# Kernel optimization log

Hardware: AMD Instinct MI355X
Metric: run time of the kernel (lower is better)

The kernel has to match this reference:

```python
import jax, jax.numpy as jnp
import numpy as np

SUB_NO = 128
T_HIST = 100
T_DATA = 20000
SYN_B = 3
HIST_B = 3
FIX_VAR = 1.0


def _build_kern(delta, log_tau, K):
    # delta: (S,), log_tau: (B,), K: (S,B) -> kernel (S, T_HIST)
    t = jnp.maximum(jnp.arange(T_HIST, dtype=jnp.float32)[None, :] - delta[:, None], 0.0)  # (S,T)
    tt = t[:, :, None] / jnp.exp(log_tau)[None, None, :]  # (S,T,B)
    return jnp.einsum('stb,sb->st', tt * jnp.exp(-tt), K)


def setup_inputs() -> dict:
    key = jax.random.key(0)
    ks = jax.random.split(key, 5)
    S = SUB_NO
    return {
        'S_conv': jax.random.normal(ks[0], (T_DATA, S), jnp.float32),
        'Y_ancest': jax.random.normal(ks[1], (T_DATA, S), jnp.float32),
        'Z_ancest': jax.random.uniform(ks[2], (T_DATA, S), jnp.float32),
        'noise': jax.random.normal(ks[3], (T_DATA, S), jnp.float32),
        'C_den': jax.random.uniform(ks[4], (S, S), jnp.float32),
        'W_sub': jnp.ones(S, jnp.float32) * 0.25,
        'theta_syn': jnp.zeros(S, jnp.float32),
        'K_spike': jnp.ones((S, SYN_B), jnp.float32) * 0.01,
        'tau_spike': jnp.arange(1.6, 1.6 + SYN_B, dtype=jnp.float32),
        'delta_spike': jnp.zeros(S, jnp.float32),
        'theta_spike': jnp.ones(S, jnp.float32) * (-1.0),
        'W_spike': jnp.ones(S, jnp.float32) * 0.1,
        'tau_hist': jnp.arange(0.5, 0.5 + HIST_B * 0.5, 0.5, dtype=jnp.float32),
        'K_hist': jnp.zeros((S, HIST_B), jnp.float32),
        'delta_hist': jnp.zeros(S, jnp.float32),
    }


def _forward(S_conv, Y_ancest, Z_ancest, noise, C_den, W_sub, theta_syn,
             K_spike, tau_spike, delta_spike, theta_spike, W_spike,
             tau_hist, K_hist, delta_hist):
    S = SUB_NO
    # kernels, flipped as in torch (conv1d cross-correlation with flipped kernel)
    hist_kf = _build_kern(delta_hist, tau_hist, K_hist)[:, ::-1]      # (S,T_HIST)
    anc_kf = _build_kern(delta_spike, tau_spike, K_spike)[:, ::-1]    # (S,T_HIST)

    # Ancestor path has no recurrence -> hoist out of the time loop.
    # spike_ancest filtering: C_den is linear & time-independent, so project first,
    # then depthwise-convolve along time.
    Z_pad = jnp.concatenate([jnp.zeros((T_HIST, S), S_conv.dtype), Z_ancest], axis=0)  # (T+T_HIST,S)
    A = Z_pad @ C_den.T  # (T+T_HIST, S)
    conv = jax.lax.conv_general_dilated(
        A.T[None],                 # (1, S, T+T_HIST)
        anc_kf[:, None, :],        # (S, 1, T_HIST)
        window_strides=(1,), padding='VALID',
        dimension_numbers=('NCH', 'OIH', 'NCH'),
        feature_group_count=S)     # (1, S, T_DATA+1)
    filtered_ancest = conv[0].T[:T_DATA]  # (T_DATA, S)

    raw_ancest = Y_ancest @ C_den.T  # (T_DATA, S)
    base = S_conv + theta_syn + filtered_ancest + raw_ancest  # (T_DATA,S)
    sqrt_var = FIX_VAR ** 0.5

    def step(buf, inp):
        # buf: (S, T_HIST) rolling history of Z_out (most recent at index -1)
        b, n = inp
        fh = jnp.sum(buf * hist_kf, axis=1)            # grouped conv1d == per-channel dot
        x_out = jax.nn.sigmoid(b + fh)
        down = x_out * W_spike + theta_spike           # down_mu_Z_t == mu_Z_t (up_mu_Z=None)
        z_out = jax.nn.sigmoid(down + n * sqrt_var)
        buf = jnp.concatenate([buf[:, 1:], z_out[:, None]], axis=1)
        return buf, (x_out * W_sub, z_out, down)

    buf0 = jnp.zeros((S, T_HIST), S_conv.dtype)
    _, (final_Y, final_Z, mu_Z) = jax.lax.scan(step, buf0, (base, noise))
    return final_Y, final_Z, mu_Z, mu_Z


def reference(S_conv, Y_ancest, Z_ancest, noise, C_den, W_sub, theta_syn,
              K_spike, tau_spike, delta_spike, theta_spike, W_spike,
              tau_hist, K_hist, delta_hist):
    return _forward(S_conv, Y_ancest, Z_ancest, noise, C_den, W_sub, theta_syn,
                    K_spike, tau_spike, delta_spike, theta_spike, W_spike,
                    tau_hist, K_hist, delta_hist)
```

## Files before the change

kernel.cpp:

```cpp
#include <hip/hip_runtime.h>

#define T_DATA 20000
#define S_NO   128
#define T_HIST 100
#define J_PAD  104
#define NELEM  (T_DATA * S_NO)

__device__ __forceinline__ float sigm(float v) {
    return 1.0f / (1.0f + __expf(-v));
}

__device__ __forceinline__ void fma4(float4& a, float s, const float4 c) {
    a.x = fmaf(s, c.x, a.x); a.y = fmaf(s, c.y, a.y);
    a.z = fmaf(s, c.z, a.z); a.w = fmaf(s, c.w, a.w);
}

__global__ void __launch_bounds__(256) k1_prep(const float* __restrict__ C,
                        const float* __restrict__ K_spike,
                        const float* __restrict__ tau_spike,
                        const float* __restrict__ delta_spike,
                        const float* __restrict__ tau_hist,
                        const float* __restrict__ K_hist,
                        const float* __restrict__ delta_hist,
                        float* __restrict__ Ct,
                        float* __restrict__ anc_kT,
                        float* __restrict__ hist_k,
                        int* __restrict__ flag) {
    const int tid = threadIdx.x;
    const int b   = blockIdx.x;
    if (b < 16) {
#pragma unroll
        for (int i = 0; i < 4; ++i) {
            const int q = b * 1024 + i * 256 + tid;
            Ct[(q & 127) * S_NO + (q >> 7)] = C[q];
        }
        return;
    }
    const int s    = tid & 127;
    const int half = tid >> 7;
    {
        float d  = delta_spike[s];
        float i0 = __expf(-tau_spike[0]);
        float i1 = __expf(-tau_spike[1]);
        float i2 = __expf(-tau_spike[2]);
        float k0 = K_spike[s * 3 + 0], k1 = K_spike[s * 3 + 1], k2 = K_spike[s * 3 + 2];
        for (int j = half * 52; j < half * 52 + 52; ++j) {
            float v = 0.0f;
            if (j < T_HIST) {
                float t  = fmaxf((float)j - d, 0.0f);
                float x0 = t * i0, x1 = t * i1, x2 = t * i2;
                v = k0 * x0 * __expf(-x0) + k1 * x1 * __expf(-x1) + k2 * x2 * __expf(-x2);
            }
            anc_kT[j * S_NO + s] = v;
        }
    }
    {
        float d  = delta_hist[s];
        float i0 = __expf(-tau_hist[0]);
        float i1 = __expf(-tau_hist[1]);
        float i2 = __expf(-tau_hist[2]);
        float k0 = K_hist[s * 3 + 0], k1 = K_hist[s * 3 + 1], k2 = K_hist[s * 3 + 2];
        for (int j = half * 50; j < half * 50 + 50; ++j) {
            float t  = fmaxf((float)j - d, 0.0f);
            float x0 = t * i0, x1 = t * i1, x2 = t * i2;
            hist_k[s * T_HIST + j] =
                k0 * x0 * __expf(-x0) + k1 * x1 * __expf(-x1) + k2 * x2 * __expf(-x2);
        }
    }
    if (tid == 0) *flag = 0;
    __syncthreads();
    if (tid < 128) {
        if (K_hist[s * 3] != 0.0f || K_hist[s * 3 + 1] != 0.0f || K_hist[s * 3 + 2] != 0.0f)
            atomicOr(flag, 1);
    }
}

__global__ void __launch_bounds__(256) k2_gemm(const float* __restrict__ Z,
                                               const float* __restrict__ Y,
                                               const float* __restrict__ Ct,
                                               float* __restrict__ A,
                                               float* __restrict__ R) {
    __shared__ float Zt[32 * 128];
    __shared__ float Yt[32 * 128];
    const int t0  = blockIdx.x * 32;
    const int tid = threadIdx.x;
    {
        const float4* Zg = (const float4*)(Z + t0 * S_NO);
        const float4* Yg = (const float4*)(Y + t0 * S_NO);
        float4* Zl = (float4*)Zt;
        float4* Yl = (float4*)Yt;
        for (int q = tid; q < 1024; q += 256) { Zl[q] = Zg[q]; Yl[q] = Yg[q]; }
    }
    __syncthreads();
    const int sg = tid & 31;
    const int tg = tid >> 5;
    const int s0 = sg * 4;
    float4 accA[4] = {{0,0,0,0},{0,0,0,0},{0,0,0,0},{0,0,0,0}};
    float4 accR[4] = {{0,0,0,0},{0,0,0,0},{0,0,0,0},{0,0,0,0}};
    for (int k4 = 0; k4 < 32; ++k4) {
        const float4 c0 = *(const float4*)&Ct[(k4 * 4 + 0) * S_NO + s0];
        const float4 c1 = *(const float4*)&Ct[(k4 * 4 + 1) * S_NO + s0];
        const float4 c2 = *(const float4*)&Ct[(k4 * 4 + 2) * S_NO + s0];
        const float4 c3 = *(const float4*)&Ct[(k4 * 4 + 3) * S_NO + s0];
#pragma unroll
        for (int i = 0; i < 4; ++i) {
            const float4 z = *(const float4*)&Zt[(tg * 4 + i) * S_NO + k4 * 4];
            fma4(accA[i], z.x, c0); fma4(accA[i], z.y, c1);
            fma4(accA[i], z.z, c2); fma4(accA[i], z.w, c3);
            const float4 y = *(const float4*)&Yt[(tg * 4 + i) * S_NO + k4 * 4];
            fma4(accR[i], y.x, c0); fma4(accR[i], y.y, c1);
            fma4(accR[i], y.z, c2); fma4(accR[i], y.w, c3);
        }
    }
#pragma unroll
    for (int i = 0; i < 4; ++i) {
        *(float4*)&A[(t0 + tg * 4 + i) * S_NO + s0] = accA[i];
        *(float4*)&R[(t0 + tg * 4 + i) * S_NO + s0] = accR[i];
    }
}

#define K3_LOGICAL 1250
#define K3_NPER    157
#define K3_PHYS    (8 * K3_NPER)

__device__ __forceinline__ void k3_fma_chunk(const float w[15], const float kj[8],
                                             float acc[8]) {
#pragma unroll
    for (int r = 0; r < 8; ++r)
#pragma unroll
        for (int i = 0; i < 8; ++i)
            acc[i] = fmaf(kj[r], w[i + 7 - r], acc[i]);
}

__device__ __forceinline__ void conv8_guard(const float* __restrict__ A,
                                            const float* __restrict__ kT,
                                            int t0, int s, float acc[8]) {
#pragma unroll 1
    for (int c = 0; c < 13; ++c) {
        const int B = t0 - 8 * c - 8;
        float w[15], kj[8];
#pragma unroll
        for (int q = 0; q < 15; ++q) {
            const int u = B + q;
            w[q] = (u >= 0) ? A[u * S_NO + s] : 0.0f;
        }
#pragma unroll
        for (int r = 0; r < 8; ++r) kj[r] = kT[(8 * c + r) * S_NO + s];
        k3_fma_chunk(w, kj, acc);
    }
}

__global__ void __launch_bounds__(256, 4) k3_fused(const float* __restrict__ A,
                                                const float* __restrict__ anc_kT,
                                                const float* __restrict__ S_conv,
                                                const float* __restrict__ noise,
                                                const float* __restrict__ W_sub,
                                                const float* __restrict__ theta_syn,
                                                const float* __restrict__ theta_spike,
                                                const float* __restrict__ W_spike,
                                                const int* __restrict__ flag,
                                                float* __restrict__ out0,
                                                float* __restrict__ out1,
                                                float* __restrict__ out2,
                                                float* __restrict__ out3,
                                                float* __restrict__ Fws) {
    const int blk = (blockIdx.x & 7) * K3_NPER + (blockIdx.x >> 3);
    if (blk >= K3_LOGICAL) return;
    const int tid = threadIdx.x;
    const int s   = tid & 127;
    const int tg  = tid >> 7;
    const int t0  = blk * 16 + tg * 8;
    const int fl  = *flag;

    float sc[8], nz[8], rr[8];
#pragma unroll
    for (int i = 0; i < 8; ++i) {
        const int n = (t0 + i) * S_NO + s;
        sc[i] = S_conv[n];
        nz[i] = noise[n];
        rr[i] = out1[n];
    }

    float acc[8] = {0,0,0,0,0,0,0,0};
    if (t0 >= J_PAD) {
        float w[15], kj[8];
        {
            const int B = t0 - 8;
#pragma unroll
            for (int q = 0; q < 15; ++q) w[q] = A[(B + q) * S_NO + s];
#pragma unroll
            for (int r = 0; r < 8; ++r) kj[r] = anc_kT[r * S_NO + s];
            k3_fma_chunk(w, kj, acc);
        }
#pragma unroll
        for (int c = 1; c < 13; ++c) {
            const int B = t0 - 8 * c - 8;
#pragma unroll
            for (int q = 6; q >= 0; --q) w[q + 8] = w[q];
#pragma unroll
            for (int q = 0; q < 8; ++q) w[q] = A[(B + q) * S_NO + s];
#pragma unroll
            for (int r = 0; r < 8; ++r) kj[r] = anc_kT[(8 * c + r) * S_NO + s];
            k3_fma_chunk(w, kj, acc);
        }
    } else {
        conv8_guard(A, anc_kT, t0, s, acc);
    }

    if (fl == 0) {
        const float tsy = theta_syn[s], wsub = W_sub[s];
        const float wsp = W_spike[s],  tsp  = theta_spike[s];
#pragma unroll
        for (int i = 0; i < 8; ++i) {
            const int n = (t0 + i) * S_NO + s;
            const float x  = sigm(sc[i] + tsy + rr[i] + acc[i]);
            const float dn = fmaf(x, wsp, tsp);
            const float z  = sigm(dn + nz[i]);
            out0[n] = x * wsub;
            out1[n] = z;
            out2[n] = dn;
            out3[n] = dn;
        }
    } else {
#pragma unroll
        for (int i = 0; i < 8; ++i) Fws[(t0 + i) * S_NO + s] = acc[i];
    }
}

__global__ void __launch_bounds__(64) k4_scan(const float* __restrict__ S_conv,
                                              const float* __restrict__ noise,
                                              const float* __restrict__ W_sub,
                                              const float* __restrict__ theta_syn,
                                              const float* __restrict__ theta_spike,
                                              const float* __restrict__ W_spike,
                                              const float* __restrict__ hist_k,
                                              const int* __restrict__ flag,
                                              const float* __restrict__ Fws,
                                              float* __restrict__ out0,
                                              float* __restrict__ out1,
                                              float* __restrict__ out2,
                                              float* __restrict__ out3) {
    if (*flag == 0) return;
    __shared__ float zr[128];
    const int s = blockIdx.x;
    const int l = threadIdx.x;
    zr[l] = 0.0f; zr[l + 64] = 0.0f;
    const float hk0 = (l < T_HIST) ? hist_k[s * T_HIST + l] : 0.0f;
    const float hk1 = (l + 64 < T_HIST) ? hist_k[s * T_HIST + l + 64] : 0.0f;
    const float tsy = theta_syn[s], wsub = W_sub[s];
    const float wsp = W_spike[s],  tsp  = theta_spike[s];
    for (int t = 0; t < T_DATA; ++t) {
        float fh = hk0 * zr[(t - 1 - l) & 127];
        fh = fmaf(hk1, zr[(t - 65 - l) & 127], fh);
#pragma unroll
        for (int m = 1; m < 64; m <<= 1) fh += __shfl_xor(fh, m, 64);
        const int n = t * S_NO + s;
        const float basev = S_conv[n] + tsy + out1[n] + Fws[n];
        const float x  = sigm(basev + fh);
        const float dn = fmaf(x, wsp, tsp);
        const float z  = sigm(dn + noise[n]);
        if (l == 0) {
            out0[n] = x * wsub;
            out1[n] = z;
            out2[n] = dn;
            out3[n] = dn;
            zr[t & 127] = z;
        }
    }
}

extern "C" void kernel_launch(void* const* d_in, const int* in_sizes, int n_in,
                              void* d_out, int out_size, void* d_ws, size_t ws_size,
                              hipStream_t stream) {
    const float* S_conv  = (const float*)d_in[0];
    const float* Y_anc   = (const float*)d_in[1];
    const float* Z_anc   = (const float*)d_in[2];
    const float* noise   = (const float*)d_in[3];
    const float* C_den   = (const float*)d_in[4];
    const float* W_sub   = (const float*)d_in[5];
    const float* th_syn  = (const float*)d_in[6];
    const float* K_spk   = (const float*)d_in[7];
    const float* tau_spk = (const float*)d_in[8];
    const float* dl_spk  = (const float*)d_in[9];
    const float* th_spk  = (const float*)d_in[10];
    const float* W_spk   = (const float*)d_in[11];
    const float* tau_h   = (const float*)d_in[12];
    const float* K_h     = (const float*)d_in[13];
    const float* dl_h    = (const float*)d_in[14];

    float* out  = (float*)d_out;
    float* out0 = out;
    float* out1 = out + NELEM;
    float* out2 = out + 2 * NELEM;
    float* out3 = out + 3 * NELEM;

    float* ws     = (float*)d_ws;
    float* wsA    = ws;
    float* wsF    = ws + NELEM;
    float* Ct     = ws + 2 * NELEM;
    float* anc_kT = Ct + S_NO * S_NO;
    float* hist_k = anc_kT + J_PAD * S_NO;
    int*   flag   = (int*)(hist_k + S_NO * T_HIST);

    k1_prep<<<17, 256, 0, stream>>>(C_den, K_spk, tau_spk, dl_spk, tau_h, K_h, dl_h,
                                    Ct, anc_kT, hist_k, flag);
    k2_gemm<<<T_DATA / 32, 256, 0, stream>>>(Z_anc, Y_anc, Ct, wsA, out1);
    k3_fused<<<K3_PHYS, 256, 0, stream>>>(wsA, anc_kT, S_conv, noise,
                                          W_sub, th_syn, th_spk, W_spk,
                                          flag, out0, out1, out2, out3, wsF);
    k4_scan<<<S_NO, 64, 0, stream>>>(S_conv, noise, W_sub, th_syn, th_spk, W_spk,
                                     hist_k, flag, wsF, out0, out1, out2, out3);
}
```

Baseline: 162.1 us.

## Store projected ancestor matrix time-major per channel for vectorized conv loads

The GEMM kernel now writes the projected ancestor matrix transposed (channel-major with padded row stride) through an LDS staging tile, and the ancestor kernel is stored per channel. The fused conv kernel then reads contiguous float4 windows along time for each channel and processes the 104-tap filter in 32-tap chunks. This replaces scalar strided loads with vector loads and larger register reuse, but each thread reads along its own row, so lane accesses are strided across rows. It also adds an extra LDS transpose pass, two more barriers and higher register pressure in the GEMM and conv kernels.

```diff
diff --git a/kernel.cpp b/kernel.cpp
--- a/kernel.cpp
+++ b/kernel.cpp
@@ -3,7 +3,7 @@
 #define T_DATA 20000
 #define S_NO   128
 #define T_HIST 100
-#define J_PAD  104
+#define ATPAD  20032
 #define NELEM  (T_DATA * S_NO)
 
 __device__ __forceinline__ float sigm(float v) {
@@ -23,7 +23,7 @@
                         const float* __restrict__ K_hist,
                         const float* __restrict__ delta_hist,
                         float* __restrict__ Ct,
-                        float* __restrict__ anc_kT,
+                        float* __restrict__ anc_kS,
                         float* __restrict__ hist_k,
                         int* __restrict__ flag) {
     const int tid = threadIdx.x;
@@ -51,7 +51,7 @@
                 float x0 = t * i0, x1 = t * i1, x2 = t * i2;
                 v = k0 * x0 * __expf(-x0) + k1 * x1 * __expf(-x1) + k2 * x2 * __expf(-x2);
             }
-            anc_kT[j * S_NO + s] = v;
+            anc_kS[s * 104 + j] = v;
         }
     }
     {
@@ -78,10 +78,11 @@
 __global__ void __launch_bounds__(256) k2_gemm(const float* __restrict__ Z,
                                                const float* __restrict__ Y,
                                                const float* __restrict__ Ct,
-                                               float* __restrict__ A,
+                                               float* __restrict__ At,
                                                float* __restrict__ R) {
-    __shared__ float Zt[32 * 128];
-    __shared__ float Yt[32 * 128];
+    __shared__ float lds[8320];
+    float* Zt = lds;
+    float* Yt = lds + 4096;
     const int t0  = blockIdx.x * 32;
     const int tid = threadIdx.x;
     {
@@ -113,9 +114,24 @@
         }
     }
 #pragma unroll
+    for (int i = 0; i < 4; ++i)
+        *(float4*)&R[(t0 + tg * 4 + i) * S_NO + s0] = accR[i];
+    __syncthreads();
+    float* Atile = lds;
+#pragma unroll
     for (int i = 0; i < 4; ++i) {
-        *(float4*)&A[(t0 + tg * 4 + i) * S_NO + s0] = accA[i];
-        *(float4*)&R[(t0 + tg * 4 + i) * S_NO + s0] = accR[i];
+        const int tl = tg * 4 + i;
+        Atile[(s0 + 0) * 33 + tl] = accA[i].x;
+        Atile[(s0 + 1) * 33 + tl] = accA[i].y;
+        Atile[(s0 + 2) * 33 + tl] = accA[i].z;
+        Atile[(s0 + 3) * 33 + tl] = accA[i].w;
+    }
+    __syncthreads();
+    for (int q = tid; q < 1024; q += 256) {
+        const int row = q >> 3, m = q & 7;
+        const float* a = &Atile[row * 33 + 4 * m];
+        const float4 v = make_float4(a[0], a[1], a[2], a[3]);
+        *(float4*)&At[row * ATPAD + t0 + 4 * m] = v;
     }
 }
 
@@ -123,35 +139,8 @@
 #define K3_NPER    157
 #define K3_PHYS    (8 * K3_NPER)
 
-__device__ __forceinline__ void k3_fma_chunk(const float w[15], const float kj[8],
-                                             float acc[8]) {
-#pragma unroll
-    for (int r = 0; r < 8; ++r)
-#pragma unroll
-        for (int i = 0; i < 8; ++i)
-            acc[i] = fmaf(kj[r], w[i + 7 - r], acc[i]);
-}
-
-__device__ __forceinline__ void conv8_guard(const float* __restrict__ A,
-                                            const float* __restrict__ kT,
-                                            int t0, int s, float acc[8]) {
-#pragma unroll 1
-    for (int c = 0; c < 13; ++c) {
-        const int B = t0 - 8 * c - 8;
-        float w[15], kj[8];
-#pragma unroll
-        for (int q = 0; q < 15; ++q) {
-            const int u = B + q;
-            w[q] = (u >= 0) ? A[u * S_NO + s] : 0.0f;
-        }
-#pragma unroll
-        for (int r = 0; r < 8; ++r) kj[r] = kT[(8 * c + r) * S_NO + s];
-        k3_fma_chunk(w, kj, acc);
-    }
-}
-
-__global__ void __launch_bounds__(256, 4) k3_fused(const float* __restrict__ A,
-                                                const float* __restrict__ anc_kT,
+__global__ void __launch_bounds__(256, 4) k3_fused(const float* __restrict__ At,
+                                                const float* __restrict__ anc_kS,
                                                 const float* __restrict__ S_conv,
                                                 const float* __restrict__ noise,
                                                 const float* __restrict__ W_sub,
@@ -181,30 +170,35 @@
         rr[i] = out1[n];
     }
 
+    const float* Arow = At + s * ATPAD;
+    const float* Krow = anc_kS + s * 104;
     float acc[8] = {0,0,0,0,0,0,0,0};
-    if (t0 >= J_PAD) {
-        float w[15], kj[8];
-        {
-            const int B = t0 - 8;
-#pragma unroll
-            for (int q = 0; q < 15; ++q) w[q] = A[(B + q) * S_NO + s];
-#pragma unroll
-            for (int r = 0; r < 8; ++r) kj[r] = anc_kT[r * S_NO + s];
-            k3_fma_chunk(w, kj, acc);
-        }
-#pragma unroll
-        for (int c = 1; c < 13; ++c) {
-            const int B = t0 - 8 * c - 8;
-#pragma unroll
-            for (int q = 6; q >= 0; --q) w[q + 8] = w[q];
-#pragma unroll
-            for (int q = 0; q < 8; ++q) w[q] = A[(B + q) * S_NO + s];
-#pragma unroll
-            for (int r = 0; r < 8; ++r) kj[r] = anc_kT[(8 * c + r) * S_NO + s];
-            k3_fma_chunk(w, kj, acc);
-        }
-    } else {
-        conv8_guard(A, anc_kT, t0, s, acc);
+#pragma unroll
+    for (int c = 0; c < 4; ++c) {
+        const int TC   = (c < 3) ? 32 : 8;
+        const int base = t0 - 32 * c - 32;
+        float w[40];
+#pragma unroll
+        for (int m = 0; m < 10; ++m) {
+            if (c == 3 && m < 6) continue;
+            const int off = base + 4 * m;
+            const float4 v = (off >= 0) ? *(const float4*)&Arow[off]
+                                        : make_float4(0.f, 0.f, 0.f, 0.f);
+            *(float4*)&w[4 * m] = v;
+        }
+        float kt[32];
+#pragma unroll
+        for (int m = 0; m < 8; ++m) {
+            if (4 * m >= TC) continue;
+            *(float4*)&kt[4 * m] = *(const float4*)&Krow[32 * c + 4 * m];
+        }
+#pragma unroll
+        for (int r = 0; r < 32; ++r) {
+            if (r >= TC) continue;
+#pragma unroll
+            for (int i = 0; i < 8; ++i)
+                acc[i] = fmaf(kt[r], w[i + 31 - r], acc[i]);
+        }
     }
 
     if (fl == 0) {
@@ -295,17 +289,17 @@
     float* out3 = out + 3 * NELEM;
 
     float* ws     = (float*)d_ws;
-    float* wsA    = ws;
-    float* wsF    = ws + NELEM;
-    float* Ct     = ws + 2 * NELEM;
-    float* anc_kT = Ct + S_NO * S_NO;
-    float* hist_k = anc_kT + J_PAD * S_NO;
+    float* At     = ws;
+    float* wsF    = At + S_NO * ATPAD;
+    float* Ct     = wsF + NELEM;
+    float* anc_kS = Ct + S_NO * S_NO;
+    float* hist_k = anc_kS + 104 * S_NO;
     int*   flag   = (int*)(hist_k + S_NO * T_HIST);
 
     k1_prep<<<17, 256, 0, stream>>>(C_den, K_spk, tau_spk, dl_spk, tau_h, K_h, dl_h,
-                                    Ct, anc_kT, hist_k, flag);
-    k2_gemm<<<T_DATA / 32, 256, 0, stream>>>(Z_anc, Y_anc, Ct, wsA, out1);
-    k3_fused<<<K3_PHYS, 256, 0, stream>>>(wsA, anc_kT, S_conv, noise,
+                                    Ct, anc_kS, hist_k, flag);
+    k2_gemm<<<T_DATA / 32, 256, 0, stream>>>(Z_anc, Y_anc, Ct, At, out1);
+    k3_fused<<<K3_PHYS, 256, 0, stream>>>(At, anc_kS, S_conv, noise,
                                           W_sub, th_syn, th_spk, W_spk,
                                           flag, out0, out1, out2, out3, wsF);
     k4_scan<<<S_NO, 64, 0, stream>>>(S_conv, noise, W_sub, th_syn, th_spk, W_spk,
```

New measurement: 287.1 us. 1.77x slower.
